# Optimization experiments

Measured on AMD Instinct MI355X. Metric: run time of the kernel, lower is better.

## Reference

```python
import jax, jax.numpy as jnp
import numpy as np

N_NODES = 40000


def gcn_conv(x, edge_index, W, b, num_nodes):
    """PyG GCNConv: add self-loops, sym-normalize, x @ W.T then scatter-add, + bias."""
    src = edge_index[0]
    dst = edge_index[1]
    loop = jnp.arange(num_nodes, dtype=src.dtype)
    src = jnp.concatenate([src, loop])
    dst = jnp.concatenate([dst, loop])
    # linear transform first (PyG applies lin before propagate)
    h = x @ W.T  # [N, out]
    # symmetric normalization: deg over destination (with self-loops)
    deg = jax.ops.segment_sum(jnp.ones_like(dst, dtype=h.dtype), dst, num_segments=num_nodes)
    dinv = jnp.where(deg > 0, jax.lax.rsqrt(deg), 0.0)
    norm = dinv[src] * dinv[dst]  # [E+N]
    msg = h[src] * norm[:, None]  # gather + scale
    out = jax.ops.segment_sum(msg, dst, num_segments=num_nodes)  # scatter-add
    return out + b


def setup_inputs() -> dict:
    key = jax.random.key(0)
    k1, k2, k3, k4, k5, k6, k7 = jax.random.split(key, 7)
    C, H, F_out = 128, 128, 1
    E = 640000
    x = jax.random.normal(k1, (N_NODES, C), dtype=jnp.float32)
    edge_index = jax.random.randint(k2, (2, E), 0, N_NODES, dtype=jnp.int64)
    # Glorot-ish init for conv weights (PyG lin.weight shape [out, in]), zero bias
    W1 = jax.random.normal(k3, (H, C), dtype=jnp.float32) / np.sqrt(C)
    b1 = jnp.zeros((H,), dtype=jnp.float32)
    W2 = jax.random.normal(k4, (F_out, H), dtype=jnp.float32) / np.sqrt(H)
    b2 = jnp.zeros((F_out,), dtype=jnp.float32)
    return {"x": x, "edge_index": edge_index, "W1": W1, "b1": b1, "W2": W2, "b2": b2}


def reference(x, edge_index, W1, b1, W2, b2):
    h = gcn_conv(x, edge_index, W1, b1, N_NODES)
    h = jax.nn.relu(h)
    out = gcn_conv(h, edge_index, W2, b2, N_NODES)
    return jax.nn.sigmoid(out)
```

## Files before the change

kernel.cpp:

```cpp
#include <hip/hip_runtime.h>
#include <math.h>
#include <stdint.h>

#define FDIM 128
#define CAP  64

typedef __bf16 bf16x8 __attribute__((ext_vector_type(8)));
typedef float  f32x4  __attribute__((ext_vector_type(4)));

__device__ __forceinline__ ushort f2bf(float f) {
    uint32_t u = __float_as_uint(f);
    uint32_t r = (u >> 16) & 1;
    return (ushort)((u + 0x7fffu + r) >> 16);
}
__device__ __forceinline__ bf16x8 pack8(float4 a, float4 b) {
    union { uint32_t q[4]; bf16x8 v; } u;
    u.q[0] = (uint32_t)f2bf(a.x) | ((uint32_t)f2bf(a.y) << 16);
    u.q[1] = (uint32_t)f2bf(a.z) | ((uint32_t)f2bf(a.w) << 16);
    u.q[2] = (uint32_t)f2bf(b.x) | ((uint32_t)f2bf(b.y) << 16);
    u.q[3] = (uint32_t)f2bf(b.z) | ((uint32_t)f2bf(b.w) << 16);
    return u.v;
}
__device__ __forceinline__ float bf_lo(uint32_t u) { return __uint_as_float(u << 16); }
__device__ __forceinline__ float bf_hi(uint32_t u) { return __uint_as_float(u & 0xFFFF0000u); }


__global__ __launch_bounds__(256) void k_prep(const float* __restrict__ W,
                                              ushort* __restrict__ Wb,
                                              int4* __restrict__ cnt4, int n4) {
    int t = blockIdx.x * blockDim.x + threadIdx.x;
    if (t < 2048) {
        int lane = t & 63, f = t >> 6;
        int jblk = f >> 2, ks = f & 3;
        int row = jblk * 16 + (lane & 15);
        int col = ks * 32 + (lane >> 4) * 8;
        const float* p = W + (size_t)row * FDIM + col;
        float4 v0 = *(const float4*)p;
        float4 v1 = *(const float4*)(p + 4);
        union { bf16x8 v; uint4 q; } u;
        u.v = pack8(v0, v1);
        *(uint4*)(Wb + (size_t)t * 8) = u.q;
    } else {
        int z = t - 2048;
        if (z < n4) cnt4[z] = make_int4(0, 0, 0, 0);
    }
}


__global__ __launch_bounds__(256) void k_scatter_ell(const int* __restrict__ src,
                                                     const int* __restrict__ dst,
                                                     int* __restrict__ cnt,
                                                     ushort* __restrict__ ell, int E) {
    int e = blockIdx.x * blockDim.x + threadIdx.x;
    if (e < E) {
        int d = dst[e];
        int p = atomicAdd(&cnt[d], 1);
        if (p < CAP) ell[(size_t)d * CAP + p] = (ushort)src[e];
    }
}


__global__ __launch_bounds__(256) void k_linear(const float* __restrict__ x,
                                                const ushort* __restrict__ Wb,
                                                const int* __restrict__ cnt,
                                                ushort* __restrict__ h, int n) {
    int tid = threadIdx.x;
    int lane = tid & 63, wid = tid >> 6;
    int mg = wid >> 1, jg2 = wid & 1;
    int node0 = (int)blockIdx.x * 64;
    int m0 = mg * 32;
    int lrow = lane & 15, kg = lane >> 4;

#pragma unroll
    for (int mt = 0; mt < 2; ++mt) {
        int row = node0 + m0 + mt * 16 + lrow;
        bool ok = (row < n);
        float s = ok ? rsqrtf((float)cnt[row] + 1.0f) : 0.f;
        const float* rp = x + (size_t)row * FDIM;
        bf16x8 af[4];
#pragma unroll
        for (int ks = 0; ks < 4; ++ks) {
            float4 v0 = make_float4(0.f, 0.f, 0.f, 0.f), v1 = v0;
            if (ok) {
                const float* p = rp + ks * 32 + kg * 8;
                v0 = *(const float4*)p;
                v1 = *(const float4*)(p + 4);
            }
            v0.x *= s; v0.y *= s; v0.z *= s; v0.w *= s;
            v1.x *= s; v1.y *= s; v1.z *= s; v1.w *= s;
            af[ks] = pack8(v0, v1);
        }
#pragma unroll
        for (int jt = 0; jt < 4; ++jt) {
            int jblk = jg2 * 4 + jt;
            f32x4 acc = {};
#pragma unroll
            for (int ks = 0; ks < 4; ++ks) {
                bf16x8 bfr = *(const bf16x8*)(Wb + ((size_t)(jblk * 4 + ks) * 64 + lane) * 8);
                acc = __builtin_amdgcn_mfma_f32_16x16x32_bf16(af[ks], bfr, acc, 0, 0, 0);
            }
            int gj = jg2 * 64 + jt * 16 + lrow;
#pragma unroll
            for (int r = 0; r < 4; ++r) {
                int gi = node0 + m0 + mt * 16 + kg * 4 + r;
                if (gi < n) h[(size_t)gi * FDIM + gj] = f2bf(acc[r]);
            }
        }
    }
}


__global__ __launch_bounds__(256) void k_agg1_h2(const uint32_t* __restrict__ h,
                                                 const ushort* __restrict__ ell,
                                                 const int* __restrict__ cnt,
                                                 const float* __restrict__ b1,
                                                 const float* __restrict__ W2,
                                                 float* __restrict__ h2s, int n) {
    int gtid = blockIdx.x * blockDim.x + threadIdx.x;
    int d = gtid >> 6;
    int lane = threadIdx.x & 63;
    if (d >= n) return;

    int degt = cnt[d];
    int deg = min(degt, CAP);
    int myidx = (lane < deg) ? (int)ell[(size_t)d * CAP + lane] : 0;

    uint32_t u = h[(size_t)d * 64 + lane];
    float ax[8], ay[8];
    ax[0] = bf_lo(u); ay[0] = bf_hi(u);
#pragma unroll
    for (int r = 1; r < 8; ++r) { ax[r] = 0.f; ay[r] = 0.f; }

    int k = 0;
    for (; k + 7 < deg; k += 8) {
        int s[8]; uint32_t uu[8];
#pragma unroll
        for (int r = 0; r < 8; ++r) s[r] = __shfl(myidx, k + r);
#pragma unroll
        for (int r = 0; r < 8; ++r) uu[r] = h[(size_t)s[r] * 64 + lane];
#pragma unroll
        for (int r = 0; r < 8; ++r) { ax[r] += bf_lo(uu[r]); ay[r] += bf_hi(uu[r]); }
    }
    for (; k + 3 < deg; k += 4) {
        int s[4]; uint32_t uu[4];
#pragma unroll
        for (int r = 0; r < 4; ++r) s[r] = __shfl(myidx, k + r);
#pragma unroll
        for (int r = 0; r < 4; ++r) uu[r] = h[(size_t)s[r] * 64 + lane];
#pragma unroll
        for (int r = 0; r < 4; ++r) { ax[r] += bf_lo(uu[r]); ay[r] += bf_hi(uu[r]); }
    }
    for (; k < deg; ++k) {
        int s0 = __shfl(myidx, k);
        uint32_t u0 = h[(size_t)s0 * 64 + lane];
        ax[0] += bf_lo(u0); ay[0] += bf_hi(u0);
    }

    float sx = ((ax[0] + ax[1]) + (ax[2] + ax[3])) + ((ax[4] + ax[5]) + (ax[6] + ax[7]));
    float sy = ((ay[0] + ay[1]) + (ay[2] + ay[3])) + ((ay[4] + ay[5]) + (ay[6] + ay[7]));

    float dd = rsqrtf((float)degt + 1.0f);
    float ox = sx * dd;
    float oy = sy * dd;

    float2 bb = *(const float2*)(b1 + lane * 2);
    float2 ww = *(const float2*)(W2 + lane * 2);
    float s = fmaxf(ox + bb.x, 0.f) * ww.x + fmaxf(oy + bb.y, 0.f) * ww.y;
#pragma unroll
    for (int o = 32; o; o >>= 1) s += __shfl_down(s, o);
    if (lane == 0) h2s[d] = s * dd;
}


__global__ __launch_bounds__(256) void k_agg2(const float* __restrict__ h2s,
                                              const ushort* __restrict__ ell,
                                              const int* __restrict__ cnt,
                                              const float* __restrict__ b2,
                                              float* __restrict__ out, int n) {
    int gtid = blockIdx.x * blockDim.x + threadIdx.x;
    int i = gtid >> 6;
    int lane = threadIdx.x & 63;
    if (i >= n) return;

    int degt = cnt[i];
    int deg = min(degt, CAP);
    float v = 0.f;
    if (lane < deg) {
        int s = ell[(size_t)i * CAP + lane];
        v = h2s[s];
    }
#pragma unroll
    for (int o = 32; o; o >>= 1) v += __shfl_down(v, o);
    if (lane == 0) {
        float dd = rsqrtf((float)degt + 1.0f);
        float r = (h2s[i] + v) * dd + b2[0];
        out[i] = 1.f / (1.f + expf(-r));
    }
}


extern "C" void kernel_launch(void* const* d_in, const int* in_sizes, int n_in,
                              void* d_out, int out_size, void* d_ws, size_t ws_size,
                              hipStream_t stream) {
    const float* x  = (const float*)d_in[0];
    const int*   ei = (const int*)d_in[1];
    const float* W1 = (const float*)d_in[2];
    const float* b1 = (const float*)d_in[3];
    const float* W2 = (const float*)d_in[4];
    const float* b2 = (const float*)d_in[5];

    int n = out_size;
    int E = in_sizes[1] / 2;
    const int* src = ei;
    const int* dst = ei + E;

    char* w = (char*)d_ws;
    int*    cnt = (int*)w;     w += (size_t)((n + 3) & ~3) * 4;
    ushort* Wb  = (ushort*)w;  w += (size_t)2048 * 8 * 2;
    ushort* ell = (ushort*)w;  w += (size_t)n * CAP * 2;
    ushort* h1s = (ushort*)w;  w += (size_t)n * FDIM * 2;
    float*  h2s = (float*)w;   w += (size_t)n * 4;

    int n4 = ((n + 3) & ~3) / 4;

    k_prep<<<(2048 + n4 + 255) / 256, 256, 0, stream>>>(W1, Wb, (int4*)cnt, n4);
    k_scatter_ell<<<(E + 255) / 256, 256, 0, stream>>>(src, dst, cnt, ell, E);
    k_linear<<<(n + 63) / 64, 256, 0, stream>>>(x, Wb, cnt, h1s, n);
    k_agg1_h2<<<(n * 64 + 255) / 256, 256, 0, stream>>>((const uint32_t*)h1s, ell, cnt, b1, W2, h2s, n);
    k_agg2<<<(n * 64 + 255) / 256, 256, 0, stream>>>(h2s, ell, cnt, b2, (float*)d_out, n);
}
```

Baseline: 87.61 us.

## Store hidden features as scaled FP8 and aggregate two nodes per wavefront

```diff
diff --git a/kernel.cpp b/kernel.cpp
--- a/kernel.cpp
+++ b/kernel.cpp
@@ -4,9 +4,11 @@
 
 #define FDIM 128
 #define CAP  64
+#define H8SCALE 8.0f
 
 typedef __bf16 bf16x8 __attribute__((ext_vector_type(8)));
 typedef float  f32x4  __attribute__((ext_vector_type(4)));
+typedef float  f32x2  __attribute__((ext_vector_type(2)));
 
 __device__ __forceinline__ ushort f2bf(float f) {
     uint32_t u = __float_as_uint(f);
@@ -21,12 +23,14 @@
     u.q[3] = (uint32_t)f2bf(b.z) | ((uint32_t)f2bf(b.w) << 16);
     return u.v;
 }
-__device__ __forceinline__ float bf_lo(uint32_t u) { return __uint_as_float(u << 16); }
-__device__ __forceinline__ float bf_hi(uint32_t u) { return __uint_as_float(u & 0xFFFF0000u); }
 
 
 __global__ __launch_bounds__(256) void k_prep(const float* __restrict__ W,
+                                              const float* __restrict__ W2,
+                                              const float* __restrict__ b1,
                                               ushort* __restrict__ Wb,
+                                              float* __restrict__ W2p,
+                                              float* __restrict__ b1p,
                                               int4* __restrict__ cnt4, int n4) {
     int t = blockIdx.x * blockDim.x + threadIdx.x;
     if (t < 2048) {
@@ -40,8 +44,14 @@
         union { bf16x8 v; uint4 q; } u;
         u.v = pack8(v0, v1);
         *(uint4*)(Wb + (size_t)t * 8) = u.q;
+    } else if (t < 2176) {
+        int i = t - 2048;
+        int q = i >> 2, tt = i & 3;
+        int c = 64 * (q >> 4) + 16 * tt + (q & 15);
+        W2p[i] = W2[c];
+        b1p[i] = b1[c];
     } else {
-        int z = t - 2048;
+        int z = t - 2176;
         if (z < n4) cnt4[z] = make_int4(0, 0, 0, 0);
     }
 }
@@ -63,7 +73,7 @@
 __global__ __launch_bounds__(256) void k_linear(const float* __restrict__ x,
                                                 const ushort* __restrict__ Wb,
                                                 const int* __restrict__ cnt,
-                                                ushort* __restrict__ h, int n) {
+                                                uint32_t* __restrict__ h8, int n) {
     int tid = threadIdx.x;
     int lane = tid & 63, wid = tid >> 6;
     int mg = wid >> 1, jg2 = wid & 1;
@@ -90,85 +100,102 @@
             v1.x *= s; v1.y *= s; v1.z *= s; v1.w *= s;
             af[ks] = pack8(v0, v1);
         }
+        f32x4 acc[4] = {};
 #pragma unroll
         for (int jt = 0; jt < 4; ++jt) {
             int jblk = jg2 * 4 + jt;
-            f32x4 acc = {};
 #pragma unroll
             for (int ks = 0; ks < 4; ++ks) {
                 bf16x8 bfr = *(const bf16x8*)(Wb + ((size_t)(jblk * 4 + ks) * 64 + lane) * 8);
-                acc = __builtin_amdgcn_mfma_f32_16x16x32_bf16(af[ks], bfr, acc, 0, 0, 0);
-            }
-            int gj = jg2 * 64 + jt * 16 + lrow;
-#pragma unroll
-            for (int r = 0; r < 4; ++r) {
-                int gi = node0 + m0 + mt * 16 + kg * 4 + r;
-                if (gi < n) h[(size_t)gi * FDIM + gj] = f2bf(acc[r]);
+                acc[jt] = __builtin_amdgcn_mfma_f32_16x16x32_bf16(af[ks], bfr, acc[jt], 0, 0, 0);
             }
         }
-    }
-}
-
-
-__global__ __launch_bounds__(256) void k_agg1_h2(const uint32_t* __restrict__ h,
+#pragma unroll
+        for (int r = 0; r < 4; ++r) {
+            int gi = node0 + m0 + mt * 16 + kg * 4 + r;
+            if (gi < n) {
+                int u = __builtin_amdgcn_cvt_pk_fp8_f32(acc[0][r] * H8SCALE,
+                                                        acc[1][r] * H8SCALE, 0, false);
+                u = __builtin_amdgcn_cvt_pk_fp8_f32(acc[2][r] * H8SCALE,
+                                                    acc[3][r] * H8SCALE, u, true);
+                h8[(size_t)gi * 32 + jg2 * 16 + lrow] = (uint32_t)u;
+            }
+        }
+    }
+}
+
+
+__global__ __launch_bounds__(256) void k_agg1_h2(const uint32_t* __restrict__ h8,
                                                  const ushort* __restrict__ ell,
                                                  const int* __restrict__ cnt,
-                                                 const float* __restrict__ b1,
-                                                 const float* __restrict__ W2,
+                                                 const float* __restrict__ b1p,
+                                                 const float* __restrict__ W2p,
                                                  float* __restrict__ h2s, int n) {
     int gtid = blockIdx.x * blockDim.x + threadIdx.x;
-    int d = gtid >> 6;
+    int wv = gtid >> 6;
     int lane = threadIdx.x & 63;
+    int half = lane >> 5;
+    int l = lane & 31;
+    int d = wv * 2 + half;
     if (d >= n) return;
 
     int degt = cnt[d];
     int deg = min(degt, CAP);
-    int myidx = (lane < deg) ? (int)ell[(size_t)d * CAP + lane] : 0;
-
-    uint32_t u = h[(size_t)d * 64 + lane];
-    float ax[8], ay[8];
-    ax[0] = bf_lo(u); ay[0] = bf_hi(u);
-#pragma unroll
-    for (int r = 1; r < 8; ++r) { ax[r] = 0.f; ay[r] = 0.f; }
+    int idxA = (l < deg) ? (int)ell[(size_t)d * CAP + l] : 0;
+    int idxB = (32 + l < deg) ? (int)ell[(size_t)d * CAP + 32 + l] : 0;
+
+    f32x4 a0 = {}, a1 = {}, a2 = {}, a3 = {};
+    {
+        uint32_t u = h8[(size_t)d * 32 + l];
+        f32x2 lo = __builtin_amdgcn_cvt_pk_f32_fp8((int)u, false);
+        f32x2 hi = __builtin_amdgcn_cvt_pk_f32_fp8((int)u, true);
+        a0[0] = lo[0]; a0[1] = lo[1]; a0[2] = hi[0]; a0[3] = hi[1];
+    }
 
     int k = 0;
-    for (; k + 7 < deg; k += 8) {
-        int s[8]; uint32_t uu[8];
-#pragma unroll
-        for (int r = 0; r < 8; ++r) s[r] = __shfl(myidx, k + r);
-#pragma unroll
-        for (int r = 0; r < 8; ++r) uu[r] = h[(size_t)s[r] * 64 + lane];
-#pragma unroll
-        for (int r = 0; r < 8; ++r) { ax[r] += bf_lo(uu[r]); ay[r] += bf_hi(uu[r]); }
-    }
     for (; k + 3 < deg; k += 4) {
-        int s[4]; uint32_t uu[4];
-#pragma unroll
-        for (int r = 0; r < 4; ++r) s[r] = __shfl(myidx, k + r);
-#pragma unroll
-        for (int r = 0; r < 4; ++r) uu[r] = h[(size_t)s[r] * 64 + lane];
-#pragma unroll
-        for (int r = 0; r < 4; ++r) { ax[r] += bf_lo(uu[r]); ay[r] += bf_hi(uu[r]); }
+        int s0 = __shfl((k + 0 < 32) ? idxA : idxB, (k + 0) & 31, 32);
+        int s1 = __shfl((k + 1 < 32) ? idxA : idxB, (k + 1) & 31, 32);
+        int s2 = __shfl((k + 2 < 32) ? idxA : idxB, (k + 2) & 31, 32);
+        int s3 = __shfl((k + 3 < 32) ? idxA : idxB, (k + 3) & 31, 32);
+        uint32_t u0 = h8[(size_t)s0 * 32 + l];
+        uint32_t u1 = h8[(size_t)s1 * 32 + l];
+        uint32_t u2 = h8[(size_t)s2 * 32 + l];
+        uint32_t u3 = h8[(size_t)s3 * 32 + l];
+        f32x2 p0 = __builtin_amdgcn_cvt_pk_f32_fp8((int)u0, false);
+        f32x2 q0 = __builtin_amdgcn_cvt_pk_f32_fp8((int)u0, true);
+        f32x2 p1 = __builtin_amdgcn_cvt_pk_f32_fp8((int)u1, false);
+        f32x2 q1 = __builtin_amdgcn_cvt_pk_f32_fp8((int)u1, true);
+        f32x2 p2 = __builtin_amdgcn_cvt_pk_f32_fp8((int)u2, false);
+        f32x2 q2 = __builtin_amdgcn_cvt_pk_f32_fp8((int)u2, true);
+        f32x2 p3 = __builtin_amdgcn_cvt_pk_f32_fp8((int)u3, false);
+        f32x2 q3 = __builtin_amdgcn_cvt_pk_f32_fp8((int)u3, true);
+        a0[0] += p0[0]; a0[1] += p0[1]; a0[2] += q0[0]; a0[3] += q0[1];
+        a1[0] += p1[0]; a1[1] += p1[1]; a1[2] += q1[0]; a1[3] += q1[1];
+        a2[0] += p2[0]; a2[1] += p2[1]; a2[2] += q2[0]; a2[3] += q2[1];
+        a3[0] += p3[0]; a3[1] += p3[1]; a3[2] += q3[0]; a3[3] += q3[1];
     }
     for (; k < deg; ++k) {
-        int s0 = __shfl(myidx, k);
-        uint32_t u0 = h[(size_t)s0 * 64 + lane];
-        ax[0] += bf_lo(u0); ay[0] += bf_hi(u0);
-    }
-
-    float sx = ((ax[0] + ax[1]) + (ax[2] + ax[3])) + ((ax[4] + ax[5]) + (ax[6] + ax[7]));
-    float sy = ((ay[0] + ay[1]) + (ay[2] + ay[3])) + ((ay[4] + ay[5]) + (ay[6] + ay[7]));
+        int s0 = __shfl((k < 32) ? idxA : idxB, k & 31, 32);
+        uint32_t u0 = h8[(size_t)s0 * 32 + l];
+        f32x2 p0 = __builtin_amdgcn_cvt_pk_f32_fp8((int)u0, false);
+        f32x2 q0 = __builtin_amdgcn_cvt_pk_f32_fp8((int)u0, true);
+        a0[0] += p0[0]; a0[1] += p0[1]; a0[2] += q0[0]; a0[3] += q0[1];
+    }
 
     float dd = rsqrtf((float)degt + 1.0f);
-    float ox = sx * dd;
-    float oy = sy * dd;
-
-    float2 bb = *(const float2*)(b1 + lane * 2);
-    float2 ww = *(const float2*)(W2 + lane * 2);
-    float s = fmaxf(ox + bb.x, 0.f) * ww.x + fmaxf(oy + bb.y, 0.f) * ww.y;
-#pragma unroll
-    for (int o = 32; o; o >>= 1) s += __shfl_down(s, o);
-    if (lane == 0) h2s[d] = s * dd;
+    float sc = dd * (1.0f / H8SCALE);
+    float4 bb = *(const float4*)(b1p + l * 4);
+    float4 ww = *(const float4*)(W2p + l * 4);
+    float o0 = (a0[0] + a1[0] + a2[0] + a3[0]) * sc;
+    float o1 = (a0[1] + a1[1] + a2[1] + a3[1]) * sc;
+    float o2 = (a0[2] + a1[2] + a2[2] + a3[2]) * sc;
+    float o3 = (a0[3] + a1[3] + a2[3] + a3[3]) * sc;
+    float s = fmaxf(o0 + bb.x, 0.f) * ww.x + fmaxf(o1 + bb.y, 0.f) * ww.y +
+              fmaxf(o2 + bb.z, 0.f) * ww.z + fmaxf(o3 + bb.w, 0.f) * ww.w;
+#pragma unroll
+    for (int o = 16; o; o >>= 1) s += __shfl_down(s, o, 32);
+    if (l == 0) h2s[d] = s * dd;
 }
 
 
@@ -215,17 +242,20 @@
     const int* dst = ei + E;
 
     char* w = (char*)d_ws;
-    int*    cnt = (int*)w;     w += (size_t)((n + 3) & ~3) * 4;
-    ushort* Wb  = (ushort*)w;  w += (size_t)2048 * 8 * 2;
-    ushort* ell = (ushort*)w;  w += (size_t)n * CAP * 2;
-    ushort* h1s = (ushort*)w;  w += (size_t)n * FDIM * 2;
-    float*  h2s = (float*)w;   w += (size_t)n * 4;
+    int*      cnt = (int*)w;      w += (size_t)((n + 3) & ~3) * 4;
+    ushort*   Wb  = (ushort*)w;   w += (size_t)2048 * 8 * 2;
+    float*    W2p = (float*)w;    w += 128 * 4;
+    float*    b1p = (float*)w;    w += 128 * 4;
+    ushort*   ell = (ushort*)w;   w += (size_t)n * CAP * 2;
+    uint32_t* h8  = (uint32_t*)w; w += (size_t)n * 32 * 4;
+    float*    h2s = (float*)w;    w += (size_t)n * 4;
 
     int n4 = ((n + 3) & ~3) / 4;
 
-    k_prep<<<(2048 + n4 + 255) / 256, 256, 0, stream>>>(W1, Wb, (int4*)cnt, n4);
+    k_prep<<<(2176 + n4 + 255) / 256, 256, 0, stream>>>(W1, W2, b1, Wb, W2p, b1p,
+                                                        (int4*)cnt, n4);
     k_scatter_ell<<<(E + 255) / 256, 256, 0, stream>>>(src, dst, cnt, ell, E);
-    k_linear<<<(n + 63) / 64, 256, 0, stream>>>(x, Wb, cnt, h1s, n);
-    k_agg1_h2<<<(n * 64 + 255) / 256, 256, 0, stream>>>((const uint32_t*)h1s, ell, cnt, b1, W2, h2s, n);
+    k_linear<<<(n + 63) / 64, 256, 0, stream>>>(x, Wb, cnt, h8, n);
+    k_agg1_h2<<<(n * 32 + 255) / 256, 256, 0, stream>>>(h8, ell, cnt, b1p, W2p, h2s, n);
     k_agg2<<<(n * 64 + 255) / 256, 256, 0, stream>>>(h2s, ell, cnt, b2, (float*)d_out, n);
 }
```

Result: faster. 80.13 us (-8.5%).
